# Kernel optimization log

Hardware: AMD Instinct MI355X
Metric: run time of the kernel (lower is better)

## Reference

```python
import jax, jax.numpy as jnp
import numpy as np

N, C_IN, T, V = 64, 64, 256, 25
C_OUT, S, MAX_N = 256, 3, 500
BN_EPS = 1e-5


def setup_inputs() -> dict:
    key = jax.random.key(0)
    ks = jax.random.split(key, 7)
    x = jax.random.normal(ks[0], (N, C_IN, T, V), dtype=jnp.float32)
    A = jax.random.uniform(ks[1], (S, V, V), dtype=jnp.float32) / V  # fixed adjacency (non-trainable buffer)
    A_pers = jax.random.normal(ks[2], (MAX_N, S, V, V), dtype=jnp.float32) * 1e-3
    # conv_branch_init: std = sqrt(2/(out*1*1*branches))
    conv_w = jax.random.normal(ks[3], (S, C_OUT, C_IN), dtype=jnp.float32) * np.sqrt(2.0 / (C_OUT * S)).astype(np.float32)
    conv_b = jax.random.normal(ks[4], (S, C_OUT), dtype=jnp.float32) * 0.01
    bn_w = jax.random.uniform(ks[5], (C_OUT,), dtype=jnp.float32) + 0.5
    bn_b = jax.random.normal(ks[6], (C_OUT,), dtype=jnp.float32) * 0.01
    return {"x": x, "A": A, "A_pers": A_pers, "conv_w": conv_w,
            "conv_b": conv_b, "bn_w": bn_w, "bn_b": bn_b}


def reference(x, A, A_pers, conv_w, conv_b, bn_w, bn_b):
    n = x.shape[0]  # n <= MAX_N
    A_personalized = jnp.tanh(A_pers[:n])          # (n, S, V, V)
    A_final = A[None] + A_personalized             # (n, S, V, V)
    # Per-sample, per-subset graph aggregation: (C*T, V) @ (V, V)
    xa = jnp.einsum('nctv,nsvw->nsctw', x, A_final)          # (n, S, C, T, V)
    # 1x1 conv per subset, summed over subsets; biases also sum over subsets
    y = jnp.einsum('nsctw,soc->notw', xa, conv_w)
    y = y + jnp.sum(conv_b, axis=0)[None, :, None, None]     # (n, C_OUT, T, V)
    # BatchNorm2d with training=True -> batch statistics (biased variance)
    mean = jnp.mean(y, axis=(0, 2, 3))
    var = jnp.var(y, axis=(0, 2, 3))
    y = (y - mean[None, :, None, None]) * (bn_w / jnp.sqrt(var + BN_EPS))[None, :, None, None] \
        + bn_b[None, :, None, None]
    y = jax.nn.relu(y)
    return (A_personalized, y)
```

## Files before the change

### kernel.cpp

```cpp
#include <hip/hip_runtime.h>
#include <math.h>

#define C_IN   64
#define T_DIM  256
#define V_DIM  25
#define C_OUT  256
#define S_DIM  3
#define BN_EPS 1e-5f

#define SC       (S_DIM * C_IN)
#define TW       (T_DIM * V_DIM)
#define AP_PER_N (S_DIM * V_DIM * V_DIM)
#define LDB      200
#define LDY      204
#define NR       32

#define NBINS    (NR * 2 * C_OUT)
#define NAP      (64 * AP_PER_N)
#define NAFB     (64 * 6 * 64 * 8)
#define NWT      (C_OUT * SC)
#define PREP_TOT (NBINS + NAP + NAFB + NWT)
#define NXU      (64 * 128 * 128 * 16)

typedef __attribute__((ext_vector_type(8))) short bf16x8;
typedef __attribute__((ext_vector_type(4))) float f32x4;

__device__ __forceinline__ unsigned short f2bf(float f) {
    unsigned u = __builtin_bit_cast(unsigned, f);
    unsigned r = u + 0x7fffu + ((u >> 16) & 1u);
    return (unsigned short)(r >> 16);
}

__device__ __forceinline__ unsigned pk_bf16(float a, float b) {
    unsigned short ul = __builtin_bit_cast(unsigned short, (__bf16)a);
    unsigned short uh = __builtin_bit_cast(unsigned short, (__bf16)b);
    return (unsigned)ul | ((unsigned)uh << 16);
}

__global__ void k_prep(const float* __restrict__ A, const float* __restrict__ A_pers,
                       const float* __restrict__ conv_w,
                       float* __restrict__ bins, float* __restrict__ out_ap,
                       unsigned short* __restrict__ afb, unsigned short* __restrict__ wt_b) {
    int i = blockIdx.x * 256 + threadIdx.x;
    if (i < NBINS) {
        bins[i] = 0.f;
        return;
    }
    i -= NBINS;
    if (i < NAP) {
        out_ap[i] = tanhf(A_pers[i]);
        return;
    }
    i -= NAP;
    if (i < NAFB) {
        int j    = i;
        int k    = j & 7;
        int lane = (j >> 3) & 63;
        int nt   = (j >> 9) & 1;
        int sn   = j >> 10;
        int s    = sn % 3;
        int n    = sn / 3;
        int v    = ((lane >> 4) << 3) + k;
        int w    = nt * 16 + (lane & 15);
        float val = 0.f;
        if (v < V_DIM && w < V_DIM)
            val = A[(s * V_DIM + v) * V_DIM + w] +
                  tanhf(A_pers[((n * S_DIM + s) * V_DIM + v) * V_DIM + w]);
        afb[j] = f2bf(val);
        return;
    }
    i -= NAFB;
    if (i < NWT) {
        int o  = i / SC;
        int sc = i - o * SC;
        int s  = sc >> 6, c = sc & 63;
        wt_b[i] = f2bf(conv_w[(s * C_OUT + o) * C_IN + c]);
    }
}

__global__ __launch_bounds__(256) void k_prepx(const float* __restrict__ x,
                                               unsigned* __restrict__ x_re) {
    int j = blockIdx.x * 256 + threadIdx.x;
    if (j >= NXU) return;
    int tile = j >> 11;
    int rem  = j & 2047;
    int row  = rem >> 4;
    int vp   = rem & 15;
    int n = tile >> 7, tp = tile & 127;
    int c = row >> 1, t = row & 1;
    const float* src = x + (size_t)n * (C_IN * TW) + (size_t)c * TW + (2 * tp + t) * V_DIM;
    int v0 = vp * 2;
    unsigned lo = (v0 < V_DIM)     ? f2bf(src[v0])     : 0;
    unsigned hi = (v0 + 1 < V_DIM) ? f2bf(src[v0 + 1]) : 0;
    x_re[j] = lo | (hi << 16);
}

template <int PASS>
__global__ __launch_bounds__(256, 3) void k_gemm(const unsigned short* __restrict__ x_re,
                                                 const unsigned short* __restrict__ afb,
                                                 const unsigned short* __restrict__ wt_b,
                                                 float* __restrict__ y,
                                                 float* __restrict__ bins,
                                                 const float2* __restrict__ ssv) {
    __shared__ __align__(16) char smem[64 * LDY * 4];
    unsigned short* sXa = (unsigned short*)smem;

    const int tid  = threadIdx.x;
    const int tp4  = blockIdx.x;
    const int nIdx = blockIdx.y;
    const int z    = blockIdx.z;
    const int lane = tid & 63;
    const int wv   = tid >> 6;
    const int l15  = lane & 15;
    const int kg   = lane >> 4;

    bf16x8 aF[6];
    {
        const unsigned short* wrow = wt_b + (size_t)(z * 64 + wv * 16 + l15) * SC + kg * 8;
#pragma unroll
        for (int ks = 0; ks < 6; ++ks)
            aF[ks] = *(const bf16x8*)(wrow + ks * 32);
    }
    bf16x8 bS[6];
    {
        const unsigned short* afbN = afb + (size_t)nIdx * (6 * 64 * 8);
#pragma unroll
        for (int sq = 0; sq < 6; ++sq)
            bS[sq] = *(const bf16x8*)(afbN + (sq * 64 + lane) * 8);
    }

    for (int j = tid; j < 2800; j += 256) {
        int u = j >= 1400, jj = j - u * 1400;
        ((unsigned*)(sXa + u * 12800))[50 * (LDB / 2) + jj] = 0;
    }

    f32x4 acc[4][4];
#pragma unroll
    for (int q = 0; q < 4; ++q)
#pragma unroll
        for (int nn = 0; nn < 4; ++nn) acc[q][nn] = (f32x4){0.f, 0.f, 0.f, 0.f};

#pragma unroll
    for (int h = 0; h < 2; ++h) {
        bf16x8 aX[2][2];
        {
            const unsigned short* xt0 = x_re + (size_t)(nIdx * 128 + tp4 * 4 + h * 2) * 4096;
#pragma unroll
            for (int u = 0; u < 2; ++u)
#pragma unroll
                for (int m2 = 0; m2 < 2; ++m2)
                    aX[u][m2] = *(const bf16x8*)(xt0 + u * 4096 + ((wv * 2 + m2) * 16 + l15) * 32 + kg * 8);
        }

#pragma unroll
        for (int sq = 0; sq < 6; ++sq) {
            int s = sq >> 1, nt = sq & 1;
            int w = nt * 16 + l15;
#pragma unroll
            for (int u = 0; u < 2; ++u) {
#pragma unroll
                for (int m2 = 0; m2 < 2; ++m2) {
                    int mt = wv * 2 + m2;
                    f32x4 c4 = __builtin_amdgcn_mfma_f32_16x16x32_bf16(
                        aX[u][m2], bS[sq], (f32x4){0.f, 0.f, 0.f, 0.f}, 0, 0, 0);
                    if (w < V_DIM) {
                        unsigned u0 = pk_bf16(c4[0], c4[2]);
                        unsigned u1 = pk_bf16(c4[1], c4[3]);
                        unsigned col = s * 32 + mt * 4 + kg;
                        unsigned* dst = (unsigned*)(sXa + u * 12800);
                        dst[w * (LDB / 2) + col]           = u0;
                        dst[(V_DIM + w) * (LDB / 2) + col] = u1;
                    }
                }
            }
        }
        __syncthreads();

#pragma unroll
        for (int ks = 0; ks < 6; ++ks) {
            bf16x8 bF[2][4];
#pragma unroll
            for (int u = 0; u < 2; ++u)
#pragma unroll
                for (int nn = 0; nn < 4; ++nn)
                    bF[u][nn] = *(const bf16x8*)(sXa + u * 12800 + (nn * 16 + l15) * LDB + ks * 32 + kg * 8);
#pragma unroll
            for (int u = 0; u < 2; ++u)
#pragma unroll
                for (int nn = 0; nn < 4; ++nn)
                    acc[h * 2 + u][nn] = __builtin_amdgcn_mfma_f32_16x16x32_bf16(
                        aF[ks], bF[u][nn], acc[h * 2 + u][nn], 0, 0, 0);
        }
        if (h == 0) __syncthreads();
    }

    const int obase = z * 64 + wv * 16;
    if (PASS == 0) {
        const int rep = (blockIdx.y * gridDim.x + blockIdx.x) & (NR - 1);
        float* b0 = bins + rep * 2 * C_OUT;
#pragma unroll
        for (int r = 0; r < 4; ++r) {
            float s1 = 0.f, s2 = 0.f;
#pragma unroll
            for (int q = 0; q < 4; ++q) {
                float v0 = acc[q][0][r], v1 = acc[q][1][r], v2 = acc[q][2][r];
                s1 += v0 + v1 + v2;
                s2 += v0 * v0 + v1 * v1 + v2 * v2;
                if (l15 < 2) {
                    float v3 = acc[q][3][r];
                    s1 += v3;
                    s2 += v3 * v3;
                }
            }
#pragma unroll
            for (int off = 1; off < 16; off <<= 1) {
                s1 += __shfl_xor(s1, off, 64);
                s2 += __shfl_xor(s2, off, 64);
            }
            if (l15 == 0) {
                int o = obase + kg * 4 + r;
                atomicAdd(&b0[o], s1);
                atomicAdd(&b0[C_OUT + o], s2);
            }
        }
    } else {
        float2 sh[4];
#pragma unroll
        for (int r = 0; r < 4; ++r)
            sh[r] = ssv[obase + kg * 4 + r];

        __syncthreads();
        float* yS = (float*)smem;
#pragma unroll
        for (int r = 0; r < 4; ++r) {
            int ol = wv * 16 + kg * 4 + r;
            float sc = sh[r].x, sf = sh[r].y;
#pragma unroll
            for (int q = 0; q < 4; ++q) {
                float* sp = yS + ol * LDY + q * 50 + l15;
                sp[0]  = fmaxf(fmaf(acc[q][0][r], sc, sf), 0.f);
                sp[16] = fmaxf(fmaf(acc[q][1][r], sc, sf), 0.f);
                sp[32] = fmaxf(fmaf(acc[q][2][r], sc, sf), 0.f);
                if (l15 < 2)
                    sp[48] = fmaxf(fmaf(acc[q][3][r], sc, sf), 0.f);
            }
        }
        __syncthreads();

        float* ydst = y + ((size_t)nIdx * C_OUT + z * 64) * TW + (size_t)tp4 * 200;
#pragma unroll
        for (int k = 0; k < 25; ++k) {
            int q = tid + k * 256;
            int o = q / 100, j2 = q - o * 100;
            float2 v = *(const float2*)(yS + o * LDY + 2 * j2);
            *(float2*)(ydst + (size_t)o * TW + 2 * j2) = v;
        }
    }
}

__global__ void k_stats(const float* __restrict__ bins, const float* __restrict__ bn_w,
                        const float* __restrict__ bn_b, float2* __restrict__ ssv, int n) {
    int o = threadIdx.x;
    float s1 = 0.f, s2 = 0.f;
    for (int rp = 0; rp < NR; ++rp) {
        s1 += bins[rp * 2 * C_OUT + o];
        s2 += bins[rp * 2 * C_OUT + C_OUT + o];
    }
    float cnt   = (float)n * (float)TW;
    float mean  = s1 / cnt;
    float var   = s2 / cnt - mean * mean;
    float scale = bn_w[o] * rsqrtf(var + BN_EPS);
    ssv[o] = make_float2(scale, bn_b[o] - mean * scale);
}

extern "C" void kernel_launch(void* const* d_in, const int* in_sizes, int n_in,
                              void* d_out, int out_size, void* d_ws, size_t ws_size,
                              hipStream_t stream) {
    const float* x      = (const float*)d_in[0];
    const float* A      = (const float*)d_in[1];
    const float* A_pers = (const float*)d_in[2];
    const float* conv_w = (const float*)d_in[3];
    const float* bn_w   = (const float*)d_in[5];
    const float* bn_b   = (const float*)d_in[6];

    const int n = in_sizes[0] / (C_IN * TW);

    float* out_ap = (float*)d_out;
    float* y      = (float*)d_out + (size_t)n * AP_PER_N;

    float*  bins = (float*)d_ws;
    float2* ssv  = (float2*)(bins + NBINS);
    unsigned short* afb  = (unsigned short*)((char*)(ssv + C_OUT));
    unsigned short* wt_b = afb + (size_t)NAFB;
    unsigned short* x_re = wt_b + (size_t)NWT;

    k_prep<<<(PREP_TOT + 255) / 256, 256, 0, stream>>>(A, A_pers, conv_w,
                                                       bins, out_ap, afb, wt_b);
    k_prepx<<<NXU / 256, 256, 0, stream>>>(x, (unsigned*)x_re);

    dim3 grid(T_DIM / 8, n, 4);
    k_gemm<0><<<grid, 256, 0, stream>>>(x_re, afb, wt_b, y, bins, ssv);
    k_stats<<<1, 256, 0, stream>>>(bins, bn_w, bn_b, ssv, n);
    k_gemm<1><<<grid, 256, 0, stream>>>(x_re, afb, wt_b, y, bins, ssv);
}
```

Baseline: 306.4 us.

## Merge prep kernels, use nontemporal output stores, raise MFMA priority

Folds the x reformatting kernel into the single prep kernel, which removes one launch. The PASS-1 BN scale/shift loads move before the GEMM loop so their latency overlaps compute. The MFMA block is wrapped in s_setprio so waves issuing matrix ops get scheduling priority. The final y writes become nontemporal float2 stores with incremental index updates instead of a per-iteration divide, aiming to avoid cache pollution on the large write-only output. Risks are longer register live ranges from hoisting the loads, and that the merged prep kernel now runs the NBINS/NAP/NAFB/NWT range checks for every x element.

```diff
diff --git a/kernel.cpp b/kernel.cpp
--- a/kernel.cpp
+++ b/kernel.cpp
@@ -21,6 +21,7 @@
 #define NWT      (C_OUT * SC)
 #define PREP_TOT (NBINS + NAP + NAFB + NWT)
 #define NXU      (64 * 128 * 128 * 16)
+#define PREP_ALL (PREP_TOT + NXU)
 
 typedef __attribute__((ext_vector_type(8))) short bf16x8;
 typedef __attribute__((ext_vector_type(4))) float f32x4;
@@ -37,10 +38,15 @@
     return (unsigned)ul | ((unsigned)uh << 16);
 }
 
+__device__ __forceinline__ void nt_store_f2(float2 v, float* p) {
+    __builtin_nontemporal_store(__builtin_bit_cast(double, v), (double*)p);
+}
+
 __global__ void k_prep(const float* __restrict__ A, const float* __restrict__ A_pers,
-                       const float* __restrict__ conv_w,
+                       const float* __restrict__ conv_w, const float* __restrict__ x,
                        float* __restrict__ bins, float* __restrict__ out_ap,
-                       unsigned short* __restrict__ afb, unsigned short* __restrict__ wt_b) {
+                       unsigned short* __restrict__ afb, unsigned short* __restrict__ wt_b,
+                       unsigned* __restrict__ x_re) {
     int i = blockIdx.x * 256 + threadIdx.x;
     if (i < NBINS) {
         bins[i] = 0.f;
@@ -75,24 +81,22 @@
         int sc = i - o * SC;
         int s  = sc >> 6, c = sc & 63;
         wt_b[i] = f2bf(conv_w[(s * C_OUT + o) * C_IN + c]);
-    }
-}
-
-__global__ __launch_bounds__(256) void k_prepx(const float* __restrict__ x,
-                                               unsigned* __restrict__ x_re) {
-    int j = blockIdx.x * 256 + threadIdx.x;
-    if (j >= NXU) return;
-    int tile = j >> 11;
-    int rem  = j & 2047;
-    int row  = rem >> 4;
-    int vp   = rem & 15;
-    int n = tile >> 7, tp = tile & 127;
-    int c = row >> 1, t = row & 1;
-    const float* src = x + (size_t)n * (C_IN * TW) + (size_t)c * TW + (2 * tp + t) * V_DIM;
-    int v0 = vp * 2;
-    unsigned lo = (v0 < V_DIM)     ? f2bf(src[v0])     : 0;
-    unsigned hi = (v0 + 1 < V_DIM) ? f2bf(src[v0 + 1]) : 0;
-    x_re[j] = lo | (hi << 16);
+        return;
+    }
+    i -= NWT;
+    if (i < NXU) {
+        int tile = i >> 11;
+        int rem  = i & 2047;
+        int row  = rem >> 4;
+        int vp   = rem & 15;
+        int n = tile >> 7, tp = tile & 127;
+        int c = row >> 1, t = row & 1;
+        const float* src = x + (size_t)n * (C_IN * TW) + (size_t)c * TW + (2 * tp + t) * V_DIM;
+        int v0 = vp * 2;
+        unsigned lo = (v0 < V_DIM)     ? f2bf(src[v0])     : 0;
+        unsigned hi = (v0 + 1 < V_DIM) ? f2bf(src[v0 + 1]) : 0;
+        x_re[i] = lo | (hi << 16);
+    }
 }
 
 template <int PASS>
@@ -113,6 +117,7 @@
     const int wv   = tid >> 6;
     const int l15  = lane & 15;
     const int kg   = lane >> 4;
+    const int obase = z * 64 + wv * 16;
 
     bf16x8 aF[6];
     {
@@ -127,6 +132,12 @@
 #pragma unroll
         for (int sq = 0; sq < 6; ++sq)
             bS[sq] = *(const bf16x8*)(afbN + (sq * 64 + lane) * 8);
+    }
+    float2 sh[4];
+    if (PASS == 1) {
+#pragma unroll
+        for (int r = 0; r < 4; ++r)
+            sh[r] = ssv[obase + kg * 4 + r];
     }
 
     for (int j = tid; j < 2800; j += 256) {
@@ -184,17 +195,18 @@
 #pragma unroll
                 for (int nn = 0; nn < 4; ++nn)
                     bF[u][nn] = *(const bf16x8*)(sXa + u * 12800 + (nn * 16 + l15) * LDB + ks * 32 + kg * 8);
+            __builtin_amdgcn_s_setprio(1);
 #pragma unroll
             for (int u = 0; u < 2; ++u)
 #pragma unroll
                 for (int nn = 0; nn < 4; ++nn)
                     acc[h * 2 + u][nn] = __builtin_amdgcn_mfma_f32_16x16x32_bf16(
                         aF[ks], bF[u][nn], acc[h * 2 + u][nn], 0, 0, 0);
+            __builtin_amdgcn_s_setprio(0);
         }
         if (h == 0) __syncthreads();
     }
 
-    const int obase = z * 64 + wv * 16;
     if (PASS == 0) {
         const int rep = (blockIdx.y * gridDim.x + blockIdx.x) & (NR - 1);
         float* b0 = bins + rep * 2 * C_OUT;
@@ -224,11 +236,6 @@
             }
         }
     } else {
-        float2 sh[4];
-#pragma unroll
-        for (int r = 0; r < 4; ++r)
-            sh[r] = ssv[obase + kg * 4 + r];
-
         __syncthreads();
         float* yS = (float*)smem;
 #pragma unroll
@@ -248,12 +255,13 @@
         __syncthreads();
 
         float* ydst = y + ((size_t)nIdx * C_OUT + z * 64) * TW + (size_t)tp4 * 200;
+        int o = tid / 100, j2 = tid - o * 100;
 #pragma unroll
         for (int k = 0; k < 25; ++k) {
-            int q = tid + k * 256;
-            int o = q / 100, j2 = q - o * 100;
             float2 v = *(const float2*)(yS + o * LDY + 2 * j2);
-            *(float2*)(ydst + (size_t)o * TW + 2 * j2) = v;
+            nt_store_f2(v, ydst + (size_t)o * TW + 2 * j2);
+            o += 2; j2 += 56;
+            if (j2 >= 100) { j2 -= 100; ++o; }
         }
     }
 }
@@ -294,9 +302,9 @@
     unsigned short* wt_b = afb + (size_t)NAFB;
     unsigned short* x_re = wt_b + (size_t)NWT;
 
-    k_prep<<<(PREP_TOT + 255) / 256, 256, 0, stream>>>(A, A_pers, conv_w,
-                                                       bins, out_ap, afb, wt_b);
-    k_prepx<<<NXU / 256, 256, 0, stream>>>(x, (unsigned*)x_re);
+    k_prep<<<(PREP_ALL + 255) / 256, 256, 0, stream>>>(A, A_pers, conv_w, x,
+                                                       bins, out_ap, afb, wt_b,
+                                                       (unsigned*)x_re);
 
     dim3 grid(T_DIM / 8, n, 4);
     k_gemm<0><<<grid, 256, 0, stream>>>(x_re, afb, wt_b, y, bins, ssv);
```

Measured after the change: 277.3 us, median of 2. -9.5%, faster.
